# Optimization experiments

Hardware: AMD Instinct MI355X
Metric: run time of the kernel (lower is better)

The kernel has to match this reference:

```python
import jax, jax.numpy as jnp
import numpy as np

DEPTH = 7  # complete binary trees with 2**DEPTH = 128 leaves

B, L = 4096, 128
V, E, OUT = 100000, 128, 3


def setup_inputs() -> dict:
    key = jax.random.key(0)
    ks = jax.random.split(key, 6)
    tokens = jax.random.randint(ks[0], (B, L), 0, V, dtype=jnp.int64)
    embedding = jax.random.normal(ks[1], (V, E), dtype=jnp.float32)
    # tree_layer: Linear(2E -> E); torch stores weight as [out, in]
    W_tree = jax.random.normal(ks[2], (E, 2 * E), dtype=jnp.float32) * (1.0 / np.sqrt(2 * E))
    b_tree = jax.random.normal(ks[3], (E,), dtype=jnp.float32) * 0.01
    # classifier_layer: Linear(E -> OUT)
    W_cls = jax.random.normal(ks[4], (OUT, E), dtype=jnp.float32) * (1.0 / np.sqrt(E))
    b_cls = jax.random.normal(ks[5], (OUT,), dtype=jnp.float32) * 0.01
    return {"tokens": tokens, "embedding": embedding, "W_tree": W_tree,
            "b_tree": b_tree, "W_cls": W_cls, "b_cls": b_cls}


def reference(tokens, embedding, W_tree, b_tree, W_cls, b_cls):
    # Leaf embeddings: gather rows of the embedding table. [B, L, E]
    reps = embedding[tokens]
    # Level-synchronous bottom-up composition (depth-batched across all trees):
    # at each level, pair adjacent nodes, concat features, apply tree_layer + tanh.
    for _ in range(DEPTH):
        left = reps[:, 0::2, :]   # [B, n/2, E]
        right = reps[:, 1::2, :]  # [B, n/2, E]
        combined = jnp.concatenate([left, right], axis=-1)  # [B, n/2, 2E]
        reps = jnp.tanh(jnp.einsum('bnh,eh->bne', combined, W_tree) + b_tree)
    roots = reps[:, 0, :]  # [B, E]
    return roots @ W_cls.T + b_cls  # [B, OUT]
```

## Files before the change

kernel.cpp:

```cpp
#include <hip/hip_runtime.h>
#include <hip/hip_fp16.h>


typedef _Float16 half8 __attribute__((ext_vector_type(8)));
typedef float floatx4 __attribute__((ext_vector_type(4)));

#define STRIDE 264
#define NPAIR 2048

__device__ __forceinline__ float fast_tanh(float x) {
  float e = __expf(2.f * x);
  return 1.f - 2.f * __builtin_amdgcn_rcpf(e + 1.f);
}

__device__ __forceinline__ unsigned pkrtz(float a, float b) {
  auto h = __builtin_amdgcn_cvt_pkrtz(a, b);
  return __builtin_bit_cast(unsigned, h);
}

__device__ __forceinline__ void mfma_k256(const _Float16* arow, const half8 (&Wf)[2][8],
                                          floatx4 (&accO)[2]) {
  floatx4 aA[2], aB[2];
  aA[0] = (floatx4){0.f, 0.f, 0.f, 0.f}; aA[1] = (floatx4){0.f, 0.f, 0.f, 0.f};
  aB[0] = (floatx4){0.f, 0.f, 0.f, 0.f}; aB[1] = (floatx4){0.f, 0.f, 0.f, 0.f};
#pragma unroll
  for (int ks = 0; ks < 4; ++ks) {
    half8 x0 = *(const half8*)(arow + ks * 32);
    half8 x1 = *(const half8*)(arow + (ks + 4) * 32);
    aA[0] = __builtin_amdgcn_mfma_f32_16x16x32_f16(x0, Wf[0][ks],     aA[0], 0, 0, 0);
    aB[0] = __builtin_amdgcn_mfma_f32_16x16x32_f16(x1, Wf[0][ks + 4], aB[0], 0, 0, 0);
    aA[1] = __builtin_amdgcn_mfma_f32_16x16x32_f16(x0, Wf[1][ks],     aA[1], 0, 0, 0);
    aB[1] = __builtin_amdgcn_mfma_f32_16x16x32_f16(x1, Wf[1][ks + 4], aB[1], 0, 0, 0);
  }
  accO[0] = aA[0] + aB[0];
  accO[1] = aA[1] + aB[1];
}

template<int MT, int MOUT, int INROW, int OUTROW, bool SPLIT, bool CLAMP8>
__device__ __forceinline__ void level_ip(
    const _Float16* inb, _Float16* outb,
    const half8 (&Wf)[2][8], const float (&bias)[2],
    int nbase, int l15, int quad)
{
  floatx4 acc[MT][2];
  if (MT == 1) {
    const int rr = CLAMP8 ? (l15 < 8 ? l15 : 7) : l15;
    mfma_k256(inb + (INROW + rr) * STRIDE + quad * 8, Wf, acc[0]);
  } else {
#pragma unroll
    for (int m = 0; m < MT; ++m) {
      acc[m][0] = (floatx4){0.f, 0.f, 0.f, 0.f};
      acc[m][1] = (floatx4){0.f, 0.f, 0.f, 0.f};
    }
#pragma unroll
    for (int m = 0; m < MT; ++m) {
      const _Float16* arow = inb + (INROW + m * 16 + l15) * STRIDE + quad * 8;
#pragma unroll
      for (int ks = 0; ks < 8; ++ks) {
        half8 a = *(const half8*)(arow + ks * 32);
        acc[m][0] = __builtin_amdgcn_mfma_f32_16x16x32_f16(a, Wf[0][ks], acc[m][0], 0, 0, 0);
        acc[m][1] = __builtin_amdgcn_mfma_f32_16x16x32_f16(a, Wf[1][ks], acc[m][1], 0, 0, 0);
      }
    }
  }

  _Float16 hv[MT][2][4];
  const int mrow = quad * 4;
#pragma unroll
  for (int m = 0; m < MT; ++m)
#pragma unroll
    for (int i = 0; i < 2; ++i)
#pragma unroll
      for (int r = 0; r < 4; ++r) {
        const int node = m * 16 + mrow + r;
        if (node < MOUT) hv[m][i][r] = (_Float16)fast_tanh(acc[m][i][r] + bias[i]);
      }

  if (SPLIT) __syncthreads();

#pragma unroll
  for (int m = 0; m < MT; ++m)
#pragma unroll
    for (int i = 0; i < 2; ++i) {
      const int col = (nbase + i) * 16 + l15;
#pragma unroll
      for (int r = 0; r < 4; ++r) {
        const int node = m * 16 + mrow + r;
        if (node < MOUT)
          outb[(OUTROW + (node >> 1)) * STRIDE + (node & 1) * 128 + col] = hv[m][i][r];
      }
    }
}

__global__ __launch_bounds__(256, 4)
void tree_kernel(const int* __restrict__ tokens,
                 const float* __restrict__ embedding,
                 const float* __restrict__ W_tree,
                 const float* __restrict__ b_tree,
                 const float* __restrict__ W_cls,
                 const float* __restrict__ b_cls,
                 float* __restrict__ out)
{
  __shared__ __align__(16) _Float16 bufA[64 * STRIDE];
  __shared__ __align__(16) _Float16 bufC[8 * STRIDE];
  __shared__ float wavepart[4][2][3];

  const int tid  = threadIdx.x;
  const int wid  = tid >> 6;
  const int lane = tid & 63;
  const int l15  = lane & 15;
  const int quad = lane >> 4;
  const int nbase = wid * 2;

  half8 Wf[2][8];
#pragma unroll
  for (int i = 0; i < 2; ++i) {
    const int e = (nbase + i) * 16 + l15;
#pragma unroll
    for (int ks = 0; ks < 8; ++ks) {
      const int k = ks * 32 + quad * 8;
      const float4* p = (const float4*)(W_tree + e * 256 + k);
      float4 lo = p[0], hi = p[1];
      half8 f;
      f[0] = (_Float16)lo.x; f[1] = (_Float16)lo.y; f[2] = (_Float16)lo.z; f[3] = (_Float16)lo.w;
      f[4] = (_Float16)hi.x; f[5] = (_Float16)hi.y; f[6] = (_Float16)hi.z; f[7] = (_Float16)hi.w;
      Wf[i][ks] = f;
    }
  }
  float bias[2];
#pragma unroll
  for (int i = 0; i < 2; ++i) bias[i] = b_tree[(nbase + i) * 16 + l15];

  float wc[2][3];
#pragma unroll
  for (int i = 0; i < 2; ++i) {
    const int col = (nbase + i) * 16 + l15;
#pragma unroll
    for (int o = 0; o < 3; ++o) wc[i][o] = W_cls[o * 128 + col];
  }

  const int leaf = tid >> 1;
  const int hh   = tid & 1;

#pragma unroll 1
  for (int p = blockIdx.x; p < NPAIR; p += gridDim.x) {

#pragma unroll 1
    for (int j = 0; j < 2; ++j) {
      const int s = 2 * p + j;
      {
        const int tok = tokens[s * 128 + leaf];
        const float4* src = (const float4*)(embedding + (size_t)tok * 128 + hh * 64);
        uint4* dst = (uint4*)bufA + (leaf >> 1) * 33 + (leaf & 1) * 16 + hh * 8;
#pragma unroll
        for (int jj = 0; jj < 8; ++jj) {
          float4 x = src[2 * jj], y = src[2 * jj + 1];
          uint4 w;
          w.x = pkrtz(x.x, x.y); w.y = pkrtz(x.z, x.w);
          w.z = pkrtz(y.x, y.y); w.w = pkrtz(y.z, y.w);
          dst[jj] = w;
        }
      }
      __syncthreads();
      level_ip<4, 64, 0,  0, true,  false>(bufA, bufA, Wf, bias, nbase, l15, quad);
      __syncthreads();
      level_ip<2, 32, 0, 32, false, false>(bufA, bufA, Wf, bias, nbase, l15, quad);
      __syncthreads();
      level_ip<1, 16, 32, 0, false, false>(bufA, bufA, Wf, bias, nbase, l15, quad);
      __syncthreads();
      level_ip<1,  8, 0,  0, false, false>(bufA, bufC + j * 4 * STRIDE, Wf, bias, nbase, l15, quad);
      __syncthreads();
    }

    level_ip<1, 8, 0, 0, false, true>(bufC, bufA, Wf, bias, nbase, l15, quad);
    __syncthreads();
    level_ip<1, 4, 0, 4, false, false>(bufA, bufA, Wf, bias, nbase, l15, quad);
    __syncthreads();

    {
      floatx4 acc[2];
      mfma_k256(bufA + (4 + l15) * STRIDE + quad * 8, Wf, acc);
      float part[2][3] = {{0.f, 0.f, 0.f}, {0.f, 0.f, 0.f}};
      if (quad == 0) {
#pragma unroll
        for (int i = 0; i < 2; ++i) {
#pragma unroll
          for (int rr = 0; rr < 2; ++rr) {
            float v = fast_tanh(acc[i][rr] + bias[i]);
#pragma unroll
            for (int o = 0; o < 3; ++o) part[rr][o] = fmaf(v, wc[i][o], part[rr][o]);
          }
        }
      }
#pragma unroll
      for (int rr = 0; rr < 2; ++rr) {
#pragma unroll
        for (int o = 0; o < 3; ++o) {
          float v = part[rr][o];
          v += __shfl_down(v, 8);
          v += __shfl_down(v, 4);
          v += __shfl_down(v, 2);
          v += __shfl_down(v, 1);
          if (lane == 0) wavepart[wid][rr][o] = v;
        }
      }
    }
    __syncthreads();
    if (tid < 6) {
      const int rr = tid / 3, o = tid - 3 * rr;
      float v = wavepart[0][rr][o] + wavepart[1][rr][o]
              + wavepart[2][rr][o] + wavepart[3][rr][o];
      out[(2 * p + rr) * 3 + o] = v + b_cls[o];
    }
  }
}

extern "C" void kernel_launch(void* const* d_in, const int* in_sizes, int n_in,
                              void* d_out, int out_size, void* d_ws, size_t ws_size,
                              hipStream_t stream) {
  const int*   tokens    = (const int*)d_in[0];
  const float* embedding = (const float*)d_in[1];
  const float* W_tree    = (const float*)d_in[2];
  const float* b_tree    = (const float*)d_in[3];
  const float* W_cls     = (const float*)d_in[4];
  const float* b_cls     = (const float*)d_in[5];
  float* out = (float*)d_out;

  dim3 grid(1024), block(256);
  tree_kernel<<<grid, block, 0, stream>>>(tokens, embedding, W_tree, b_tree, W_cls, b_cls, out);
}
```

Before: 160.2 us.

## Feed leaf level MFMA directly from global embedding rows, skip LDS staging

The first tree level now loads embedding rows straight from global memory into MFMA operand registers, packing them to fp16 in-register instead of first staging all 128 leaves in shared memory. This removes one LDS write/read pass and one barrier per tree, and shrinks the shared buffer. The cost is that each wave re-fetches the same embedding rows (every wave loads all leaves for its own column slice), which multiplies global/L2 traffic. The occupancy hint drops from 4 to 2 blocks per SM, and the split-barrier path is removed.

```diff
diff --git a/kernel.cpp b/kernel.cpp
--- a/kernel.cpp
+++ b/kernel.cpp
@@ -16,6 +16,13 @@
 __device__ __forceinline__ unsigned pkrtz(float a, float b) {
   auto h = __builtin_amdgcn_cvt_pkrtz(a, b);
   return __builtin_bit_cast(unsigned, h);
+}
+
+__device__ __forceinline__ half8 pack8(float4 a, float4 b) {
+  uint4 u;
+  u.x = pkrtz(a.x, a.y); u.y = pkrtz(a.z, a.w);
+  u.z = pkrtz(b.x, b.y); u.w = pkrtz(b.z, b.w);
+  return __builtin_bit_cast(half8, u);
 }
 
 __device__ __forceinline__ void mfma_k256(const _Float16* arow, const half8 (&Wf)[2][8],
@@ -36,7 +43,7 @@
   accO[1] = aA[1] + aB[1];
 }
 
-template<int MT, int MOUT, int INROW, int OUTROW, bool SPLIT, bool CLAMP8>
+template<int MT, int MOUT, int INROW, int OUTROW, bool CLAMP8>
 __device__ __forceinline__ void level_ip(
     const _Float16* inb, _Float16* outb,
     const half8 (&Wf)[2][8], const float (&bias)[2],
@@ -64,35 +71,66 @@
     }
   }
 
-  _Float16 hv[MT][2][4];
   const int mrow = quad * 4;
 #pragma unroll
   for (int m = 0; m < MT; ++m)
 #pragma unroll
-    for (int i = 0; i < 2; ++i)
+    for (int i = 0; i < 2; ++i) {
+      const int col = (nbase + i) * 16 + l15;
 #pragma unroll
       for (int r = 0; r < 4; ++r) {
         const int node = m * 16 + mrow + r;
-        if (node < MOUT) hv[m][i][r] = (_Float16)fast_tanh(acc[m][i][r] + bias[i]);
-      }
-
-  if (SPLIT) __syncthreads();
-
-#pragma unroll
-  for (int m = 0; m < MT; ++m)
+        if (node < MOUT) {
+          float v = fast_tanh(acc[m][i][r] + bias[i]);
+          outb[(OUTROW + (node >> 1)) * STRIDE + (node & 1) * 128 + col] = (_Float16)v;
+        }
+      }
+    }
+}
+
+__device__ __forceinline__ void l0_direct(
+    const int* __restrict__ tokS, const float* __restrict__ emb, _Float16* outb,
+    const half8 (&Wf)[2][8], const float (&bias)[2],
+    int nbase, int l15, int quad)
+{
+#pragma unroll 1
+  for (int m = 0; m < 4; ++m) {
+    const int2 tk = *(const int2*)(tokS + 32 * m + 2 * l15);
+    const float* b0 = emb + (size_t)tk.x * 128 + quad * 8;
+    const float* b1 = emb + (size_t)tk.y * 128 + quad * 8;
+    floatx4 aA[2], aB[2];
+    aA[0] = (floatx4){0.f, 0.f, 0.f, 0.f}; aA[1] = (floatx4){0.f, 0.f, 0.f, 0.f};
+    aB[0] = (floatx4){0.f, 0.f, 0.f, 0.f}; aB[1] = (floatx4){0.f, 0.f, 0.f, 0.f};
+#pragma unroll
+    for (int ks = 0; ks < 4; ++ks) {
+      float4 x0 = *(const float4*)(b0 + ks * 32);
+      float4 x1 = *(const float4*)(b0 + ks * 32 + 4);
+      float4 y0 = *(const float4*)(b1 + ks * 32);
+      float4 y1 = *(const float4*)(b1 + ks * 32 + 4);
+      half8 hx = pack8(x0, x1);
+      half8 hy = pack8(y0, y1);
+      aA[0] = __builtin_amdgcn_mfma_f32_16x16x32_f16(hx, Wf[0][ks],     aA[0], 0, 0, 0);
+      aB[0] = __builtin_amdgcn_mfma_f32_16x16x32_f16(hy, Wf[0][ks + 4], aB[0], 0, 0, 0);
+      aA[1] = __builtin_amdgcn_mfma_f32_16x16x32_f16(hx, Wf[1][ks],     aA[1], 0, 0, 0);
+      aB[1] = __builtin_amdgcn_mfma_f32_16x16x32_f16(hy, Wf[1][ks + 4], aB[1], 0, 0, 0);
+    }
+    floatx4 acc[2] = {aA[0] + aB[0], aA[1] + aB[1]};
+
+    const int mrow = quad * 4;
 #pragma unroll
     for (int i = 0; i < 2; ++i) {
       const int col = (nbase + i) * 16 + l15;
 #pragma unroll
       for (int r = 0; r < 4; ++r) {
         const int node = m * 16 + mrow + r;
-        if (node < MOUT)
-          outb[(OUTROW + (node >> 1)) * STRIDE + (node & 1) * 128 + col] = hv[m][i][r];
-      }
-    }
-}
-
-__global__ __launch_bounds__(256, 4)
+        float v = fast_tanh(acc[i][r] + bias[i]);
+        outb[(node >> 1) * STRIDE + (node & 1) * 128 + col] = (_Float16)v;
+      }
+    }
+  }
+}
+
+__global__ __launch_bounds__(256, 2)
 void tree_kernel(const int* __restrict__ tokens,
                  const float* __restrict__ embedding,
                  const float* __restrict__ W_tree,
@@ -101,7 +139,7 @@
                  const float* __restrict__ b_cls,
                  float* __restrict__ out)
 {
-  __shared__ __align__(16) _Float16 bufA[64 * STRIDE];
+  __shared__ __align__(16) _Float16 bufA[48 * STRIDE];
   __shared__ __align__(16) _Float16 bufC[8 * STRIDE];
   __shared__ float wavepart[4][2][3];
 
@@ -139,42 +177,25 @@
     for (int o = 0; o < 3; ++o) wc[i][o] = W_cls[o * 128 + col];
   }
 
-  const int leaf = tid >> 1;
-  const int hh   = tid & 1;
-
 #pragma unroll 1
   for (int p = blockIdx.x; p < NPAIR; p += gridDim.x) {
 
 #pragma unroll 1
     for (int j = 0; j < 2; ++j) {
       const int s = 2 * p + j;
-      {
-        const int tok = tokens[s * 128 + leaf];
-        const float4* src = (const float4*)(embedding + (size_t)tok * 128 + hh * 64);
-        uint4* dst = (uint4*)bufA + (leaf >> 1) * 33 + (leaf & 1) * 16 + hh * 8;
-#pragma unroll
-        for (int jj = 0; jj < 8; ++jj) {
-          float4 x = src[2 * jj], y = src[2 * jj + 1];
-          uint4 w;
-          w.x = pkrtz(x.x, x.y); w.y = pkrtz(x.z, x.w);
-          w.z = pkrtz(y.x, y.y); w.w = pkrtz(y.z, y.w);
-          dst[jj] = w;
-        }
-      }
-      __syncthreads();
-      level_ip<4, 64, 0,  0, true,  false>(bufA, bufA, Wf, bias, nbase, l15, quad);
-      __syncthreads();
-      level_ip<2, 32, 0, 32, false, false>(bufA, bufA, Wf, bias, nbase, l15, quad);
-      __syncthreads();
-      level_ip<1, 16, 32, 0, false, false>(bufA, bufA, Wf, bias, nbase, l15, quad);
-      __syncthreads();
-      level_ip<1,  8, 0,  0, false, false>(bufA, bufC + j * 4 * STRIDE, Wf, bias, nbase, l15, quad);
-      __syncthreads();
-    }
-
-    level_ip<1, 8, 0, 0, false, true>(bufC, bufA, Wf, bias, nbase, l15, quad);
+      l0_direct(tokens + s * 128, embedding, bufA, Wf, bias, nbase, l15, quad);
+      __syncthreads();
+      level_ip<2, 32, 0, 32, false>(bufA, bufA, Wf, bias, nbase, l15, quad);
+      __syncthreads();
+      level_ip<1, 16, 32, 0, false>(bufA, bufA, Wf, bias, nbase, l15, quad);
+      __syncthreads();
+      level_ip<1,  8, 0,  0, false>(bufA, bufC + j * 4 * STRIDE, Wf, bias, nbase, l15, quad);
+      __syncthreads();
+    }
+
+    level_ip<1, 8, 0, 0, true>(bufC, bufA, Wf, bias, nbase, l15, quad);
     __syncthreads();
-    level_ip<1, 4, 0, 4, false, false>(bufA, bufA, Wf, bias, nbase, l15, quad);
+    level_ip<1, 4, 0, 4, false>(bufA, bufA, Wf, bias, nbase, l15, quad);
     __syncthreads();
 
     {
```

Result: slower. 241.5 us (+50.7%).
